# Kernel optimization log

Hardware: AMD Instinct MI355X
Metric: run time of the kernel (lower is better)

The kernel has to match this reference:

```python
import jax, jax.numpy as jnp
import numpy as np

N = 50000
E = 1600000
F_IN = 256
DIMS = 64
N_CLS = 16
R = 8


def glorot(key, shape):
    fan = shape[-2] + shape[-1] if len(shape) >= 2 else shape[-1] * 2
    std = jnp.sqrt(6.0 / fan)
    return jax.random.uniform(key, shape, jnp.float32, -std, std)


def setup_inputs() -> dict:
    key = jax.random.key(0)
    ks = jax.random.split(key, 12)
    x = jax.random.normal(ks[0], (N, F_IN), jnp.float32)
    edge_index = jax.random.randint(ks[1], (2, E), 0, N)
    edge_weight = jax.random.uniform(ks[2], (E,), jnp.float32)
    edge_color = jax.random.randint(ks[3], (E,), 0, R)
    W1 = glorot(ks[4], (R, F_IN, DIMS))
    atten1 = glorot(ks[5], (R, 2 * DIMS))
    root1 = glorot(ks[6], (F_IN, DIMS))
    bias1 = jnp.zeros((DIMS,), jnp.float32)
    W2 = glorot(ks[7], (R, DIMS, N_CLS))
    atten2 = glorot(ks[8], (R, 2 * N_CLS))
    root2 = glorot(ks[9], (DIMS, N_CLS))
    bias2 = jnp.zeros((N_CLS,), jnp.float32)
    return dict(x=x, edge_index=edge_index, edge_weight=edge_weight,
                edge_color=edge_color, W1=W1, atten1=atten1, root1=root1,
                bias1=bias1, W2=W2, atten2=atten2, root2=root2, bias2=bias2)


def wrgat_conv(x, src, dst, ew, ec, W, atten, root, bias):
    # x: [N, f_in]; W: [R, f_in, d]; atten: [R, 2d]
    d = W.shape[-1]
    xr = jnp.einsum('nf,rfd->rnd', x, W)            # [R, N, d] per-relation projection
    xi = xr[ec, dst]                                 # [E, d] dst (x_i)
    xj = xr[ec, src]                                 # [E, d] src (x_j)
    a_i = atten[:, :d][ec]                           # [E, d]
    a_j = atten[:, d:][ec]
    s = jnp.sum(a_i * xi + a_j * xj, axis=-1)        # [E]
    s = jax.nn.leaky_relu(s, 0.2)
    # segment softmax over (relation, destination) groups
    seg = ec * N + dst                               # [E], each edge belongs to one relation
    nseg = R * N
    m = jax.ops.segment_max(s, seg, num_segments=nseg)
    m = jnp.where(jnp.isfinite(m), m, 0.0)           # empty segments -> 0
    e = jnp.exp(s - m[seg])
    denom = jax.ops.segment_sum(e, seg, num_segments=nseg)
    alpha = e / jnp.maximum(denom[seg], 1e-16)
    msg = (alpha * ew)[:, None] * xj                 # [E, d]
    summed = jax.ops.segment_sum(msg, seg, num_segments=nseg).reshape(R, N, d)
    cnt = jax.ops.segment_sum(jnp.ones_like(ew), seg, num_segments=nseg).reshape(R, N, 1)
    out = (summed / jnp.maximum(cnt, 1.0)).sum(axis=0)  # mean aggr per relation, summed over relations
    return out + x @ root + bias


def reference(x, edge_index, edge_weight, edge_color, W1, atten1, root1, bias1,
              W2, atten2, root2, bias2):
    src, dst = edge_index[0], edge_index[1]          # PyG flow source_to_target: x_j=src, x_i=dst
    h = wrgat_conv(x, src, dst, edge_weight, edge_color, W1, atten1, root1, bias1)
    h = jax.nn.relu(h)                               # dropout p=0 -> identity
    h = wrgat_conv(h, src, dst, edge_weight, edge_color, W2, atten2, root2, bias2)
    return jax.nn.log_softmax(h, axis=1)
```

## Files before the change

kernel.cpp:

```cpp
#include <hip/hip_runtime.h>
#include <math.h>

#define N_NODES 50000
#define N_EDGES 1600000
#define F_IN    256
#define DIMS    64
#define N_CLS   16
#define R_REL   8
#define CAP     96

#define PROJ_BLKS 3519
#define CSR_BLKS  6250
#define FRONT_BLKS (PROJ_BLKS + CSR_BLKS)

typedef short bf16x8 __attribute__((ext_vector_type(8)));
typedef float f32x4  __attribute__((ext_vector_type(4)));
typedef unsigned int u32;
typedef const __attribute__((address_space(1))) u32* gas_ptr;
typedef __attribute__((address_space(3))) u32* las_ptr;

__device__ __forceinline__ void async16(const void* g, void* l) {
    __builtin_amdgcn_global_load_lds((gas_ptr)g, (las_ptr)l, 16, 0, 0);
}

__device__ __forceinline__ unsigned short f2bf(float f) {
    unsigned u = __float_as_uint(f);
    unsigned r = (u + 0x7fffu + ((u >> 16) & 1u)) >> 16;
    return (unsigned short)r;
}
__device__ __forceinline__ float bf2f(unsigned short u) {
    return __uint_as_float(((unsigned)u) << 16);
}

__global__ __launch_bounds__(256) void cvt_x_kernel(
        const float* __restrict__ x, ushort* __restrict__ xb) {
    int i4 = blockIdx.x * 256 + threadIdx.x;
    float4 v = ((const float4*)x)[i4];
    ushort4 o;
    o.x = f2bf(v.x); o.y = f2bf(v.y); o.z = f2bf(v.z); o.w = f2bf(v.w);
    ((ushort4*)xb)[i4] = o;
}

__global__ __launch_bounds__(256) void cvt_w_kernel(
        const float* __restrict__ W1, const float* __restrict__ root1,
        ushort* __restrict__ wt1) {
    int idx = blockIdx.x * 256 + threadIdx.x;
    int r = idx >> 14, rem = idx & 16383;
    int n = rem >> 8, k = rem & 255;
    float v = (r < 8) ? W1[((size_t)r * F_IN + k) * DIMS + n]
                      : root1[(size_t)k * DIMS + n];
    wt1[idx] = f2bf(v);
}

#define BM 128
__global__ __launch_bounds__(256, 6) void front_kernel(
        const ushort* __restrict__ xb, const ushort* __restrict__ wt1,
        const float* __restrict__ at1,
        ushort* __restrict__ xr1b, float* __restrict__ hroot,
        float* __restrict__ si1, float* __restrict__ sj1,
        const int* __restrict__ ei, const int* __restrict__ ecol,
        const float* __restrict__ ew, int* __restrict__ fill,
        unsigned long long* __restrict__ rec) {
    __shared__ ushort xs[BM * 64];
    const int bid = blockIdx.x;
    const int t = threadIdx.x;

    int pb = -1, cb = -1;
    if (bid < 2 * PROJ_BLKS) { if (bid & 1) cb = bid >> 1; else pb = bid >> 1; }
    else cb = PROJ_BLKS + (bid - 2 * PROJ_BLKS);

    if (cb >= 0) {
        int e = cb * 256 + t;
        int s = ei[e], d = ei[N_EDGES + e], c = ecol[e];
        float w_ = ew[e];
        int p = atomicAdd(&fill[d], 1);
        int idx = (p < CAP) ? d * CAP + p : N_NODES * CAP;
        unsigned long long rv =
            ((unsigned long long)__float_as_uint(w_) << 32)
            | (unsigned)(s | (c << 16));
        __builtin_nontemporal_store(rv, &rec[idx]);
        return;
    }

    const int r = pb / 391;
    const int node0 = (pb % 391) * BM;
    const ushort* wrow = wt1 + (size_t)r * 64 * 256;

    const int w = t >> 6, lane = t & 63;
    const int lane15 = lane & 15, quad = lane >> 4;
    const int row0 = w * 32 + lane15;
    const int sw0 = row0 & 7;

    f32x4 acc[2][4];
    #pragma unroll
    for (int a = 0; a < 2; ++a)
        #pragma unroll
        for (int b = 0; b < 4; ++b)
            acc[a][b] = (f32x4){0.f, 0.f, 0.f, 0.f};

    for (int s = 0; s < 4; ++s) {
        __syncthreads();
        #pragma unroll
        for (int c = 0; c < 4; ++c) {
            int slot = c * 256 + t;
            int row = slot >> 3, k8p = slot & 7;
            int k8 = k8p ^ (row & 7);
            int node = node0 + row;
            if (node >= N_NODES) node = N_NODES - 1;
            async16(&xb[(size_t)node * 256 + s * 64 + k8 * 8],
                    &xs[(c * 256 + w * 64) * 8]);
        }
        __syncthreads();
        #pragma unroll
        for (int kk = 0; kk < 2; ++kk) {
            int k8 = kk * 4 + quad;
            int aidx = row0 * 64 + ((k8 ^ sw0) << 3);
            bf16x8 a0 = *(const bf16x8*)&xs[aidx];
            bf16x8 a1 = *(const bf16x8*)&xs[aidx + 16 * 64];
            int kg = s * 64 + kk * 32 + quad * 8;
            #pragma unroll
            for (int nt = 0; nt < 4; ++nt) {
                bf16x8 b = *(const bf16x8*)&wrow[(size_t)(nt * 16 + lane15) * 256 + kg];
                acc[0][nt] = __builtin_amdgcn_mfma_f32_16x16x32_bf16(a0, b, acc[0][nt], 0, 0, 0);
                acc[1][nt] = __builtin_amdgcn_mfma_f32_16x16x32_bf16(a1, b, acc[1][nt], 0, 0, 0);
            }
        }
    }

    const float* at = at1 + r * 128;
    #pragma unroll
    for (int mt = 0; mt < 2; ++mt) {
        float pi[4] = {0.f, 0.f, 0.f, 0.f};
        float pj[4] = {0.f, 0.f, 0.f, 0.f};
        #pragma unroll
        for (int nt = 0; nt < 4; ++nt) {
            int gcol = nt * 16 + lane15;
            float ai = 0.f, aj = 0.f;
            if (r < 8) { ai = at[gcol]; aj = at[64 + gcol]; }
            #pragma unroll
            for (int reg = 0; reg < 4; ++reg) {
                float v = acc[mt][nt][reg];
                int grow = node0 + w * 32 + mt * 16 + quad * 4 + reg;
                if (grow < N_NODES) {
                    if (r < 8)
                        xr1b[((size_t)r * N_NODES + grow) * 64 + gcol] = f2bf(v);
                    else
                        hroot[(size_t)grow * 64 + gcol] = v;
                }
                pi[reg] += ai * v;
                pj[reg] += aj * v;
            }
        }
        if (r < 8) {
            #pragma unroll
            for (int reg = 0; reg < 4; ++reg) {
                float s_ = pi[reg], u_ = pj[reg];
                #pragma unroll
                for (int off = 1; off < 16; off <<= 1) {
                    s_ += __shfl_xor(s_, off, 64);
                    u_ += __shfl_xor(u_, off, 64);
                }
                if (lane15 == 0) {
                    int grow = node0 + w * 32 + mt * 16 + quad * 4 + reg;
                    if (grow < N_NODES) {
                        si1[r * N_NODES + grow] = s_;
                        sj1[r * N_NODES + grow] = u_;
                    }
                }
            }
        }
    }
}

__global__ __launch_bounds__(256) void agg1s_kernel(
        const unsigned long long* __restrict__ rec, const int* __restrict__ fill,
        const float* __restrict__ si, const float* __restrict__ sj,
        const ushort* __restrict__ xr1b, const float* __restrict__ hroot,
        const float* __restrict__ bias1, float* __restrict__ h) {
    __shared__ int   esrc[4][CAP];
    __shared__ float ecoef[4][CAP];
    __shared__ float sden[4][8];
    __shared__ int   scnt[4][8];
    __shared__ float ssi[4][8];
    const int t = threadIdx.x;
    const int w = t >> 6, lane = t & 63;
    const int d = blockIdx.x * 4 + w;
    if (lane < 8) {
        sden[w][lane] = 0.f; scnt[w][lane] = 0;
        ssi[w][lane] = si[lane * N_NODES + d];
    }
    const int n = min(fill[d], CAP);
    const int base = d * CAP;
    float ex[2] = {0.f, 0.f}, ww[2] = {0.f, 0.f};
    int cc[2] = {0, 0};
    #pragma unroll
    for (int ii = 0; ii < 2; ++ii) {
        int i = lane + ii * 64;
        if (i < n) {
            unsigned long long rv = rec[base + i];
            int px = (int)(unsigned)rv;
            int s = px & 0xffff, c = (px >> 16) & 0x7fff;
            esrc[w][i] = px;
            float sc = ssi[w][c] + sj[c * N_NODES + s];
            sc = sc > 0.f ? sc : 0.2f * sc;
            float e = __expf(sc);
            ex[ii] = e; cc[ii] = c; ww[ii] = __uint_as_float((unsigned)(rv >> 32));
            atomicAdd(&sden[w][c], e);
            atomicAdd(&scnt[w][c], 1);
        }
    }
    #pragma unroll
    for (int ii = 0; ii < 2; ++ii) {
        int i = lane + ii * 64;
        if (i < n)
            ecoef[w][i] = ex[ii] / fmaxf(sden[w][cc[ii]], 1e-16f)
                          * ww[ii] / (float)scnt[w][cc[ii]];
    }
    float a0 = 0.f, a1 = 0.f, a2 = 0.f, a3 = 0.f;
    int i = 0;
    for (; i + 4 <= n; i += 4) {
        int p0 = esrc[w][i], p1 = esrc[w][i + 1];
        int p2 = esrc[w][i + 2], p3 = esrc[w][i + 3];
        float c0 = ecoef[w][i], c1 = ecoef[w][i + 1];
        float c2 = ecoef[w][i + 2], c3 = ecoef[w][i + 3];
        int r0 = (p0 >> 16) * N_NODES + (p0 & 0xffff);
        int r1 = (p1 >> 16) * N_NODES + (p1 & 0xffff);
        int r2 = (p2 >> 16) * N_NODES + (p2 & 0xffff);
        int r3 = (p3 >> 16) * N_NODES + (p3 & 0xffff);
        a0 += c0 * bf2f(xr1b[(size_t)r0 * 64 + lane]);
        a1 += c1 * bf2f(xr1b[(size_t)r1 * 64 + lane]);
        a2 += c2 * bf2f(xr1b[(size_t)r2 * 64 + lane]);
        a3 += c3 * bf2f(xr1b[(size_t)r3 * 64 + lane]);
    }
    for (; i < n; ++i) {
        int p0 = esrc[w][i];
        int r0 = (p0 >> 16) * N_NODES + (p0 & 0xffff);
        a0 += ecoef[w][i] * bf2f(xr1b[(size_t)r0 * 64 + lane]);
    }
    float acc = (a0 + a1) + (a2 + a3) + hroot[(size_t)d * 64 + lane] + bias1[lane];
    h[(size_t)d * 64 + lane] = fmaxf(acc, 0.f);
}

__global__ __launch_bounds__(256) void proj2_kernel(
        const float* __restrict__ h, const float* __restrict__ W2,
        const float* __restrict__ atten2, ushort* __restrict__ xr2b,
        float* __restrict__ si2, float* __restrict__ sj2) {
    __shared__ float w2sh[8][64][16];
    __shared__ float a2sh[8][32];
    __shared__ float hsh[32][65];
    const int t = threadIdx.x;
    for (int i = t; i < R_REL * DIMS * N_CLS; i += 256)
        w2sh[i >> 10][(i >> 4) & 63][i & 15] = W2[i];
    if (t < R_REL * 2 * N_CLS) a2sh[t >> 5][t & 31] = atten2[t];
    const int node0 = blockIdx.x * 32;
    for (int i = t; i < 32 * 64; i += 256) {
        int nn = i >> 6, kk = i & 63;
        int node = node0 + nn;
        hsh[nn][kk] = (node < N_NODES) ? h[(size_t)node * 64 + kk] : 0.f;
    }
    __syncthreads();
    const int nl = t & 31, r = t >> 5;
    const int node = node0 + nl;
    float acc[16] = {};
    #pragma unroll 4
    for (int k = 0; k < 64; ++k) {
        float hv = hsh[nl][k];
        #pragma unroll
        for (int c = 0; c < 16; ++c) acc[c] += hv * w2sh[r][k][c];
    }
    if (node < N_NODES) {
        float si = 0.f, sj = 0.f;
        size_t base = ((size_t)r * N_NODES + node) * 16;
        #pragma unroll
        for (int c = 0; c < 16; ++c) {
            si += a2sh[r][c] * acc[c];
            sj += a2sh[r][16 + c] * acc[c];
        }
        #pragma unroll
        for (int c4 = 0; c4 < 4; ++c4) {
            ushort4 o;
            o.x = f2bf(acc[c4 * 4 + 0]); o.y = f2bf(acc[c4 * 4 + 1]);
            o.z = f2bf(acc[c4 * 4 + 2]); o.w = f2bf(acc[c4 * 4 + 3]);
            *(ushort4*)&xr2b[base + c4 * 4] = o;
        }
        si2[r * N_NODES + node] = si;
        sj2[r * N_NODES + node] = sj;
    }
}

__global__ __launch_bounds__(256) void agg2s_kernel(
        const unsigned long long* __restrict__ rec, const int* __restrict__ fill,
        const float* __restrict__ si, const float* __restrict__ sj,
        const ushort* __restrict__ xr2b, const float* __restrict__ h,
        const float* __restrict__ root2, const float* __restrict__ bias2,
        float* __restrict__ out) {
    __shared__ float rsh[64][17];
    __shared__ float hsh[4][64];
    __shared__ int   esrc[4][CAP];
    __shared__ float ecoef[4][CAP];
    __shared__ float sden[4][8];
    __shared__ int   scnt[4][8];
    __shared__ float ssi[4][8];
    const int t = threadIdx.x;
    for (int i = t; i < DIMS * N_CLS; i += 256) rsh[i >> 4][i & 15] = root2[i];
    const int w = t >> 6, lane = t & 63;
    const int d = blockIdx.x * 4 + w;
    hsh[w][lane] = h[(size_t)d * 64 + lane];
    if (lane < 8) {
        sden[w][lane] = 0.f; scnt[w][lane] = 0;
        ssi[w][lane] = si[lane * N_NODES + d];
    }
    const int n = min(fill[d], CAP);
    const int base = d * CAP;
    float ex[2] = {0.f, 0.f}, ww[2] = {0.f, 0.f};
    int cc[2] = {0, 0};
    #pragma unroll
    for (int ii = 0; ii < 2; ++ii) {
        int i = lane + ii * 64;
        if (i < n) {
            unsigned long long rv = rec[base + i];
            int px = (int)(unsigned)rv;
            int s = px & 0xffff, c = (px >> 16) & 0x7fff;
            esrc[w][i] = px;
            float sc = ssi[w][c] + sj[c * N_NODES + s];
            sc = sc > 0.f ? sc : 0.2f * sc;
            float e = __expf(sc);
            ex[ii] = e; cc[ii] = c; ww[ii] = __uint_as_float((unsigned)(rv >> 32));
            atomicAdd(&sden[w][c], e);
            atomicAdd(&scnt[w][c], 1);
        }
    }
    #pragma unroll
    for (int ii = 0; ii < 2; ++ii) {
        int i = lane + ii * 64;
        if (i < n)
            ecoef[w][i] = ex[ii] / fmaxf(sden[w][cc[ii]], 1e-16f)
                          * ww[ii] / (float)scnt[w][cc[ii]];
    }
    __syncthreads();
    const int sub = lane >> 4, cd = lane & 15;
    float acc = 0.f;
    for (int i = sub; i < n; i += 4) {
        int p = esrc[w][i];
        int row = (p >> 16) * N_NODES + (p & 0xffff);
        acc += ecoef[w][i] * bf2f(xr2b[(size_t)row * 16 + cd]);
    }
    #pragma unroll
    for (int k0 = 0; k0 < 16; ++k0) {
        int k = sub * 16 + k0;
        acc += hsh[w][k] * rsh[k][cd];
    }
    acc += __shfl_xor(acc, 16, 64);
    acc += __shfl_xor(acc, 32, 64);
    if (sub == 0) {
        acc += bias2[cd];
        float m = acc;
        #pragma unroll
        for (int off = 8; off; off >>= 1) m = fmaxf(m, __shfl_xor(m, off, 16));
        float ex2 = expf(acc - m);
        float ssum = ex2;
        #pragma unroll
        for (int off = 8; off; off >>= 1) ssum += __shfl_xor(ssum, off, 16);
        out[(size_t)d * 16 + cd] = acc - m - logf(ssum);
    }
}

extern "C" void kernel_launch(void* const* d_in, const int* in_sizes, int n_in,
                              void* d_out, int out_size, void* d_ws, size_t ws_size,
                              hipStream_t stream) {
    const float* x     = (const float*)d_in[0];
    const int*   ei    = (const int*)  d_in[1];
    const float* ew    = (const float*)d_in[2];
    const int*   ecol  = (const int*)  d_in[3];
    const float* W1    = (const float*)d_in[4];
    const float* at1   = (const float*)d_in[5];
    const float* root1 = (const float*)d_in[6];
    const float* b1    = (const float*)d_in[7];
    const float* W2    = (const float*)d_in[8];
    const float* at2   = (const float*)d_in[9];
    const float* root2 = (const float*)d_in[10];
    const float* b2    = (const float*)d_in[11];
    float* out = (float*)d_out;
    float* ws  = (float*)d_ws;

    ushort*   xb    = (ushort*)(ws + 0);
    ushort*   wt1   = (ushort*)(ws + 6400000);
    ushort*   xr1b  = (ushort*)(ws + 6480000);
    float*    hroot = ws + 19280000;
    ushort*   xr2b  = (ushort*)(ws + 22480000);
    float*    si1   = ws + 25680000;
    float*    sj1   = ws + 26080000;
    float*    si2   = ws + 26480000;
    float*    sj2   = ws + 26880000;
    int*      fill  = (int*)(ws + 27280000);
    float*    h     = ws + 27330000;
    unsigned long long* rec = (unsigned long long*)(ws + 30530000);

    hipMemsetAsync(fill, 0, (size_t)N_NODES * 4, stream);

    cvt_x_kernel<<<12500, 256, 0, stream>>>(x, xb);
    cvt_w_kernel<<<576, 256, 0, stream>>>(W1, root1, wt1);
    front_kernel<<<FRONT_BLKS, 256, 0, stream>>>(xb, wt1, at1, xr1b, hroot,
                                                 si1, sj1, ei, ecol, ew, fill, rec);
    agg1s_kernel<<<12500, 256, 0, stream>>>(rec, fill, si1, sj1, xr1b, hroot, b1, h);
    proj2_kernel<<<1563, 256, 0, stream>>>(h, W2, at2, xr2b, si2, sj2);
    agg2s_kernel<<<12500, 256, 0, stream>>>(rec, fill, si2, sj2, xr2b, h, root2, b2, out);
}
```

Baseline: 421.6 us.

## Fuse layer-2 projection into aggregation, merge prep kernels, store root and h in bf16

Merges the x and W conversion kernels into one prep kernel that also builds half of the CSR edge records, so edge bucketing overlaps the conversion work. The other half stays interleaved with the layer-1 projection. The layer-2 projection and its attention scores are now computed inside the layer-1 aggregation kernel straight from the just-computed h row, which removes the separate proj2 launch and the h round trip. The root term and h are stored in bf16 to cut bytes moved, at some cost in precision. The fused per-node projection reads W2 from global memory per lane instead of through shared memory.

```diff
diff --git a/kernel.cpp b/kernel.cpp
--- a/kernel.cpp
+++ b/kernel.cpp
@@ -9,9 +9,12 @@
 #define R_REL   8
 #define CAP     96
 
+#define CVT_BLKS  12500
+#define CSRH      3125
+#define CVTW_BLKS 576
+#define PREP_BLKS (CVT_BLKS + CSRH + CVTW_BLKS)
 #define PROJ_BLKS 3519
-#define CSR_BLKS  6250
-#define FRONT_BLKS (PROJ_BLKS + CSR_BLKS)
+#define FRONT_BLKS (PROJ_BLKS + CSRH)
 
 typedef short bf16x8 __attribute__((ext_vector_type(8)));
 typedef float f32x4  __attribute__((ext_vector_type(4)));
@@ -32,31 +35,55 @@
     return __uint_as_float(((unsigned)u) << 16);
 }
 
-__global__ __launch_bounds__(256) void cvt_x_kernel(
-        const float* __restrict__ x, ushort* __restrict__ xb) {
-    int i4 = blockIdx.x * 256 + threadIdx.x;
-    float4 v = ((const float4*)x)[i4];
-    ushort4 o;
-    o.x = f2bf(v.x); o.y = f2bf(v.y); o.z = f2bf(v.z); o.w = f2bf(v.w);
-    ((ushort4*)xb)[i4] = o;
-}
-
-__global__ __launch_bounds__(256) void cvt_w_kernel(
+__device__ __forceinline__ void csr_edge(
+        int e, const int* __restrict__ ei, const int* __restrict__ ecol,
+        const float* __restrict__ ew, int* __restrict__ fill,
+        unsigned long long* __restrict__ rec) {
+    int s = ei[e], d = ei[N_EDGES + e], c = ecol[e];
+    float w_ = ew[e];
+    int p = atomicAdd(&fill[d], 1);
+    int idx = (p < CAP) ? d * CAP + p : N_NODES * CAP;
+    unsigned long long rv =
+        ((unsigned long long)__float_as_uint(w_) << 32)
+        | (unsigned)(s | (c << 16));
+    __builtin_nontemporal_store(rv, &rec[idx]);
+}
+
+__global__ __launch_bounds__(256) void prep_kernel(
+        const float* __restrict__ x, ushort* __restrict__ xb,
         const float* __restrict__ W1, const float* __restrict__ root1,
-        ushort* __restrict__ wt1) {
-    int idx = blockIdx.x * 256 + threadIdx.x;
-    int r = idx >> 14, rem = idx & 16383;
-    int n = rem >> 8, k = rem & 255;
-    float v = (r < 8) ? W1[((size_t)r * F_IN + k) * DIMS + n]
-                      : root1[(size_t)k * DIMS + n];
-    wt1[idx] = f2bf(v);
+        ushort* __restrict__ wt1,
+        const int* __restrict__ ei, const int* __restrict__ ecol,
+        const float* __restrict__ ew, int* __restrict__ fill,
+        unsigned long long* __restrict__ rec) {
+    const int bid = blockIdx.x;
+    const int t = threadIdx.x;
+    if (bid < CVT_BLKS + CSRH) {
+        int g = bid / 5, m = bid - g * 5;
+        if (m == 4) {
+            csr_edge(g * 256 + t, ei, ecol, ew, fill, rec);
+        } else {
+            int i4 = (g * 4 + m) * 256 + t;
+            float4 v = ((const float4*)x)[i4];
+            ushort4 o;
+            o.x = f2bf(v.x); o.y = f2bf(v.y); o.z = f2bf(v.z); o.w = f2bf(v.w);
+            ((ushort4*)xb)[i4] = o;
+        }
+    } else {
+        int idx = (bid - (CVT_BLKS + CSRH)) * 256 + t;
+        int r = idx >> 14, rem = idx & 16383;
+        int n = rem >> 8, k = rem & 255;
+        float v = (r < 8) ? W1[((size_t)r * F_IN + k) * DIMS + n]
+                          : root1[(size_t)k * DIMS + n];
+        wt1[idx] = f2bf(v);
+    }
 }
 
 #define BM 128
 __global__ __launch_bounds__(256, 6) void front_kernel(
         const ushort* __restrict__ xb, const ushort* __restrict__ wt1,
         const float* __restrict__ at1,
-        ushort* __restrict__ xr1b, float* __restrict__ hroot,
+        ushort* __restrict__ xr1b, ushort* __restrict__ hrootb,
         float* __restrict__ si1, float* __restrict__ sj1,
         const int* __restrict__ ei, const int* __restrict__ ecol,
         const float* __restrict__ ew, int* __restrict__ fill,
@@ -66,19 +93,11 @@
     const int t = threadIdx.x;
 
     int pb = -1, cb = -1;
-    if (bid < 2 * PROJ_BLKS) { if (bid & 1) cb = bid >> 1; else pb = bid >> 1; }
-    else cb = PROJ_BLKS + (bid - 2 * PROJ_BLKS);
+    if (bid < 2 * CSRH) { if (bid & 1) cb = bid >> 1; else pb = bid >> 1; }
+    else pb = CSRH + (bid - 2 * CSRH);
 
     if (cb >= 0) {
-        int e = cb * 256 + t;
-        int s = ei[e], d = ei[N_EDGES + e], c = ecol[e];
-        float w_ = ew[e];
-        int p = atomicAdd(&fill[d], 1);
-        int idx = (p < CAP) ? d * CAP + p : N_NODES * CAP;
-        unsigned long long rv =
-            ((unsigned long long)__float_as_uint(w_) << 32)
-            | (unsigned)(s | (c << 16));
-        __builtin_nontemporal_store(rv, &rec[idx]);
+        csr_edge(800000 + cb * 256 + t, ei, ecol, ew, fill, rec);
         return;
     }
 
@@ -145,7 +164,7 @@
                     if (r < 8)
                         xr1b[((size_t)r * N_NODES + grow) * 64 + gcol] = f2bf(v);
                     else
-                        hroot[(size_t)grow * 64 + gcol] = v;
+                        hrootb[(size_t)grow * 64 + gcol] = f2bf(v);
                 }
                 pi[reg] += ai * v;
                 pj[reg] += aj * v;
@@ -175,10 +194,14 @@
 __global__ __launch_bounds__(256) void agg1s_kernel(
         const unsigned long long* __restrict__ rec, const int* __restrict__ fill,
         const float* __restrict__ si, const float* __restrict__ sj,
-        const ushort* __restrict__ xr1b, const float* __restrict__ hroot,
-        const float* __restrict__ bias1, float* __restrict__ h) {
+        const ushort* __restrict__ xr1b, const ushort* __restrict__ hrootb,
+        const float* __restrict__ bias1, ushort* __restrict__ hb,
+        const float* __restrict__ W2, const float* __restrict__ at2,
+        ushort* __restrict__ xr2b, float* __restrict__ si2,
+        float* __restrict__ sj2) {
     __shared__ int   esrc[4][CAP];
     __shared__ float ecoef[4][CAP];
+    __shared__ float hval[4][64];
     __shared__ float sden[4][8];
     __shared__ int   scnt[4][8];
     __shared__ float ssi[4][8];
@@ -237,61 +260,38 @@
         int r0 = (p0 >> 16) * N_NODES + (p0 & 0xffff);
         a0 += ecoef[w][i] * bf2f(xr1b[(size_t)r0 * 64 + lane]);
     }
-    float acc = (a0 + a1) + (a2 + a3) + hroot[(size_t)d * 64 + lane] + bias1[lane];
-    h[(size_t)d * 64 + lane] = fmaxf(acc, 0.f);
-}
-
-__global__ __launch_bounds__(256) void proj2_kernel(
-        const float* __restrict__ h, const float* __restrict__ W2,
-        const float* __restrict__ atten2, ushort* __restrict__ xr2b,
-        float* __restrict__ si2, float* __restrict__ sj2) {
-    __shared__ float w2sh[8][64][16];
-    __shared__ float a2sh[8][32];
-    __shared__ float hsh[32][65];
-    const int t = threadIdx.x;
-    for (int i = t; i < R_REL * DIMS * N_CLS; i += 256)
-        w2sh[i >> 10][(i >> 4) & 63][i & 15] = W2[i];
-    if (t < R_REL * 2 * N_CLS) a2sh[t >> 5][t & 31] = atten2[t];
-    const int node0 = blockIdx.x * 32;
-    for (int i = t; i < 32 * 64; i += 256) {
-        int nn = i >> 6, kk = i & 63;
-        int node = node0 + nn;
-        hsh[nn][kk] = (node < N_NODES) ? h[(size_t)node * 64 + kk] : 0.f;
-    }
-    __syncthreads();
-    const int nl = t & 31, r = t >> 5;
-    const int node = node0 + nl;
-    float acc[16] = {};
-    #pragma unroll 4
+    float hf = (a0 + a1) + (a2 + a3)
+               + bf2f(hrootb[(size_t)d * 64 + lane]) + bias1[lane];
+    hf = fmaxf(hf, 0.f);
+    hb[(size_t)d * 64 + lane] = f2bf(hf);
+    hval[w][lane] = hf;
+    const int r_ = lane >> 4, c_ = lane & 15;
+    float v0 = 0.f, v1 = 0.f;
+    #pragma unroll 8
     for (int k = 0; k < 64; ++k) {
-        float hv = hsh[nl][k];
-        #pragma unroll
-        for (int c = 0; c < 16; ++c) acc[c] += hv * w2sh[r][k][c];
-    }
-    if (node < N_NODES) {
-        float si = 0.f, sj = 0.f;
-        size_t base = ((size_t)r * N_NODES + node) * 16;
-        #pragma unroll
-        for (int c = 0; c < 16; ++c) {
-            si += a2sh[r][c] * acc[c];
-            sj += a2sh[r][16 + c] * acc[c];
-        }
-        #pragma unroll
-        for (int c4 = 0; c4 < 4; ++c4) {
-            ushort4 o;
-            o.x = f2bf(acc[c4 * 4 + 0]); o.y = f2bf(acc[c4 * 4 + 1]);
-            o.z = f2bf(acc[c4 * 4 + 2]); o.w = f2bf(acc[c4 * 4 + 3]);
-            *(ushort4*)&xr2b[base + c4 * 4] = o;
-        }
-        si2[r * N_NODES + node] = si;
-        sj2[r * N_NODES + node] = sj;
+        float hk = hval[w][k];
+        v0 += hk * W2[((size_t)r_ * 64 + k) * 16 + c_];
+        v1 += hk * W2[((size_t)(r_ + 4) * 64 + k) * 16 + c_];
+    }
+    xr2b[((size_t)r_ * N_NODES + d) * 16 + c_] = f2bf(v0);
+    xr2b[((size_t)(r_ + 4) * N_NODES + d) * 16 + c_] = f2bf(v1);
+    float s0 = at2[r_ * 32 + c_] * v0,        j0 = at2[r_ * 32 + 16 + c_] * v0;
+    float s1 = at2[(r_ + 4) * 32 + c_] * v1,  j1 = at2[(r_ + 4) * 32 + 16 + c_] * v1;
+    #pragma unroll
+    for (int off = 1; off < 16; off <<= 1) {
+        s0 += __shfl_xor(s0, off, 64); j0 += __shfl_xor(j0, off, 64);
+        s1 += __shfl_xor(s1, off, 64); j1 += __shfl_xor(j1, off, 64);
+    }
+    if (c_ == 0) {
+        si2[r_ * N_NODES + d] = s0;       sj2[r_ * N_NODES + d] = j0;
+        si2[(r_ + 4) * N_NODES + d] = s1; sj2[(r_ + 4) * N_NODES + d] = j1;
     }
 }
 
 __global__ __launch_bounds__(256) void agg2s_kernel(
         const unsigned long long* __restrict__ rec, const int* __restrict__ fill,
         const float* __restrict__ si, const float* __restrict__ sj,
-        const ushort* __restrict__ xr2b, const float* __restrict__ h,
+        const ushort* __restrict__ xr2b, const ushort* __restrict__ hb,
         const float* __restrict__ root2, const float* __restrict__ bias2,
         float* __restrict__ out) {
     __shared__ float rsh[64][17];
@@ -305,7 +305,7 @@
     for (int i = t; i < DIMS * N_CLS; i += 256) rsh[i >> 4][i & 15] = root2[i];
     const int w = t >> 6, lane = t & 63;
     const int d = blockIdx.x * 4 + w;
-    hsh[w][lane] = h[(size_t)d * 64 + lane];
+    hsh[w][lane] = bf2f(hb[(size_t)d * 64 + lane]);
     if (lane < 8) {
         sden[w][lane] = 0.f; scnt[w][lane] = 0;
         ssi[w][lane] = si[lane * N_NODES + d];
@@ -386,23 +386,24 @@
     ushort*   xb    = (ushort*)(ws + 0);
     ushort*   wt1   = (ushort*)(ws + 6400000);
     ushort*   xr1b  = (ushort*)(ws + 6480000);
-    float*    hroot = ws + 19280000;
-    ushort*   xr2b  = (ushort*)(ws + 22480000);
-    float*    si1   = ws + 25680000;
-    float*    sj1   = ws + 26080000;
-    float*    si2   = ws + 26480000;
-    float*    sj2   = ws + 26880000;
-    int*      fill  = (int*)(ws + 27280000);
-    float*    h     = ws + 27330000;
-    unsigned long long* rec = (unsigned long long*)(ws + 30530000);
+    ushort*   hrootb= (ushort*)(ws + 19280000);
+    ushort*   xr2b  = (ushort*)(ws + 20880000);
+    float*    si1   = ws + 24080000;
+    float*    sj1   = ws + 24480000;
+    float*    si2   = ws + 24880000;
+    float*    sj2   = ws + 25280000;
+    int*      fill  = (int*)(ws + 25680000);
+    ushort*   hb    = (ushort*)(ws + 25730000);
+    unsigned long long* rec = (unsigned long long*)(ws + 27330000);
 
     hipMemsetAsync(fill, 0, (size_t)N_NODES * 4, stream);
 
-    cvt_x_kernel<<<12500, 256, 0, stream>>>(x, xb);
-    cvt_w_kernel<<<576, 256, 0, stream>>>(W1, root1, wt1);
-    front_kernel<<<FRONT_BLKS, 256, 0, stream>>>(xb, wt1, at1, xr1b, hroot,
+    prep_kernel<<<PREP_BLKS, 256, 0, stream>>>(x, xb, W1, root1, wt1,
+                                               ei, ecol, ew, fill, rec);
+    front_kernel<<<FRONT_BLKS, 256, 0, stream>>>(xb, wt1, at1, xr1b, hrootb,
                                                  si1, sj1, ei, ecol, ew, fill, rec);
-    agg1s_kernel<<<12500, 256, 0, stream>>>(rec, fill, si1, sj1, xr1b, hroot, b1, h);
-    proj2_kernel<<<1563, 256, 0, stream>>>(h, W2, at2, xr2b, si2, sj2);
-    agg2s_kernel<<<12500, 256, 0, stream>>>(rec, fill, si2, sj2, xr2b, h, root2, b2, out);
-}
+    agg1s_kernel<<<12500, 256, 0, stream>>>(rec, fill, si1, sj1, xr1b, hrootb,
+                                            b1, hb, W2, at2, xr2b, si2, sj2);
+    agg2s_kernel<<<12500, 256, 0, stream>>>(rec, fill, si2, sj2, xr2b, hb,
+                                            root2, b2, out);
+}
```

Result: slower. 463.2 us (+9.9%).
